# Kernel tuning notes

Measured on AMD Instinct MI355X. Metric: run time of the kernel, lower is better.

## Reference

```python
import jax, jax.numpy as jnp
import numpy as np

N = 8192
IN_FEATS = 256
D = IN_FEATS // 4  # 64, bottleneck dim
HID = 64           # MLP hidden_dim
K_MAX = 9
K_EC = 20
SLOPE = 0.01       # torch LeakyReLU default


def _leaky(x):
    return jnp.where(x >= 0, x, SLOPE * x)


def _knn_idx(f, k):
    # f: [N, d]; returns [N, k] indices of k nearest (incl. self, dist 0), ascending distance
    sq = jnp.sum(f * f, axis=1)
    dist = sq[:, None] + sq[None, :] - 2.0 * (f @ f.T)  # [N, N]
    _, idx = jax.lax.top_k(-dist, k)
    return idx


def _edge_conv(f, idx, Wt, bt, Wp, bp, W1, b1, W2, b2):
    # f: [N, d]; idx: [N, k] neighbor (src) indices; dst is the row node.
    x_nb = f[idx]                                   # [N, k, d] gather of src feats
    theta = (f[:, None, :] - x_nb) @ Wt.T + bt      # v_sub_u -> theta Linear
    phi = f @ Wp.T + bp                             # [N, d]
    z = phi[:, None, :] + theta                     # [N, k, d]
    # MLP(hidden=64, 2 layers, leaky_relu, activation_first=True)
    z = _leaky(z) @ W1.T + b1
    z = _leaky(z) @ W2.T + b2
    return jnp.max(z, axis=1)                       # max aggregation per dst


def _lin_init(key, out_dim, in_dim):
    k1, k2 = jax.random.split(key)
    bound = 1.0 / np.sqrt(in_dim)
    W = jax.random.uniform(k1, (out_dim, in_dim), jnp.float32, -bound, bound)
    b = jax.random.uniform(k2, (out_dim,), jnp.float32, -bound, bound)
    return W, b


def setup_inputs() -> dict:
    key = jax.random.key(0)
    keys = jax.random.split(key, 12)
    inp = {"feature": jax.random.normal(keys[0], (N, IN_FEATS), jnp.float32)}
    inp["Wb"], inp["bb"] = _lin_init(keys[1], D, IN_FEATS)
    inp["Wt1"], inp["bt1"] = _lin_init(keys[2], D, D)
    inp["Wp1"], inp["bp1"] = _lin_init(keys[3], D, D)
    inp["Wm1a"], inp["bm1a"] = _lin_init(keys[4], HID, D)
    inp["Wm1b"], inp["bm1b"] = _lin_init(keys[5], D, HID)
    inp["Wt2"], inp["bt2"] = _lin_init(keys[6], D, D)
    inp["Wp2"], inp["bp2"] = _lin_init(keys[7], D, D)
    inp["Wm2a"], inp["bm2a"] = _lin_init(keys[8], HID, D)
    inp["Wm2b"], inp["bm2b"] = _lin_init(keys[9], D, HID)
    inp["Wl"], inp["bl"] = _lin_init(keys[10], IN_FEATS, 3 * D)
    return inp


def reference(feature, Wb, bb, Wt1, bt1, Wp1, bp1, Wm1a, bm1a, Wm1b, bm1b,
              Wt2, bt2, Wp2, bp2, Wm2a, bm2a, Wm2b, bm2b, Wl, bl):
    f = feature @ Wb.T + bb                          # bottleneck [N, D]
    # KNN indices are non-differentiable (torch topk indices) -> stop_gradient
    idx40 = _knn_idx(jax.lax.stop_gradient(f), K_EC * 2)  # 40-NN, ascending distance
    idx9 = idx40[:, :K_MAX]
    idx20 = idx40[:, :K_EC]            # dilation 1
    idx20_d2 = idx40[:, ::2]           # dilation 2: every 2nd of 40-NN
    h_max = jnp.max(f[idx9], axis=1)   # copy_u + max over 9-NN
    h1 = _edge_conv(f, idx20, Wt1, bt1, Wp1, bp1, Wm1a, bm1a, Wm1b, bm1b)
    h2 = _edge_conv(f, idx20_d2, Wt2, bt2, Wp2, bp2, Wm2a, bm2a, Wm2b, bm2b)
    h = jnp.concatenate([h1, h2, h_max], axis=1) @ Wl.T + bl
    return h + feature                 # residual
```

## Files before the change

### kernel.cpp

```cpp
#include <hip/hip_runtime.h>
#include <math.h>

#define NPT   8192
#define FIN   256
#define DD    64
#define KSEL  48
#define QT    16

#define LEAKY(x) (((x) >= 0.f) ? (x) : 0.01f*(x))

using short8v = __attribute__((ext_vector_type(8))) short;
using f32x4   = __attribute__((ext_vector_type(4))) float;

__device__ inline unsigned short f2bf(float x) {
  union { float f; unsigned u; } v; v.f = x;
  unsigned r = v.u + 0x7fff + ((v.u >> 16) & 1);
  return (unsigned short)(r >> 16);
}
__device__ inline float bf2f(unsigned short h) {
  union { unsigned u; float f; } v; v.u = ((unsigned)h) << 16; return v.f;
}

__device__ __forceinline__ void sort_merge(float& ld, int& li, float sd, int si, int l) {
  #pragma unroll
  for (int k = 2; k <= 64; k <<= 1) {
    #pragma unroll
    for (int j = k >> 1; j >= 1; j >>= 1) {
      float pd = __shfl_xor(sd, j);
      int   pi = __shfl_xor(si, j);
      bool up = ((l & k) == 0);
      bool lower = ((l & j) == 0);
      bool takeMin = (up == lower);
      bool pick = takeMin ? (pd < sd) : (pd > sd);
      sd = pick ? pd : sd;
      si = pick ? pi : si;
    }
  }
  float rd = __shfl(sd, 63 - l);
  int   ri = __shfl(si, 63 - l);
  bool keep = (ld <= rd);
  float md = keep ? ld : rd;
  int   mi = keep ? li : ri;
  #pragma unroll
  for (int j = 32; j >= 1; j >>= 1) {
    float pd = __shfl_xor(md, j);
    int   pi = __shfl_xor(mi, j);
    bool lower = ((l & j) == 0);
    bool pick = lower ? (pd < md) : (pd > md);
    md = pick ? pd : md;
    mi = pick ? pi : mi;
  }
  ld = md; li = mi;
}

__global__ void k0_prep(const float* __restrict__ Wl, const float* __restrict__ Wb,
                        const float* __restrict__ Wt1, const float* __restrict__ Wp1,
                        const float* __restrict__ Wt2, const float* __restrict__ Wp2,
                        float* __restrict__ WlT, float* __restrict__ WbT,
                        float* __restrict__ WtT1, float* __restrict__ WpT1,
                        float* __restrict__ WtT2, float* __restrict__ WpT2)
{
  const int b = blockIdx.x, t = threadIdx.x;
  if (b < 192) {
    WlT[b*256 + t] = Wl[t*192 + b];
  } else if (b < 256) {
    int j = (b - 192)*4 + (t >> 6), o = t & 63;
    WbT[j*64 + o] = Wb[o*256 + j];
  } else {
    int m = b - 256;
    const float* src = (m==0) ? Wt1 : (m==1) ? Wp1 : (m==2) ? Wt2 : Wp2;
    float*       dst = (m==0) ? WtT1: (m==1) ? WpT1: (m==2) ? WtT2: WpT2;
    #pragma unroll
    for (int i = 0; i < 16; ++i) {
      int idx = t + 256*i, r = idx >> 6, c = idx & 63;
      dst[c*64 + r] = src[r*64 + c];
    }
  }
}

__global__ __launch_bounds__(256) void k1_precompute(
    const float* __restrict__ feature, const float* __restrict__ WbT, const float* __restrict__ bb,
    const float* __restrict__ WtT1, const float* __restrict__ bt1,
    const float* __restrict__ WpT1, const float* __restrict__ bp1,
    const float* __restrict__ WtT2, const float* __restrict__ bt2,
    const float* __restrict__ WpT2, const float* __restrict__ bp2,
    double* __restrict__ f64d, double* __restrict__ sq64,
    float* __restrict__ f32v, float* __restrict__ sqf,
    float* __restrict__ u1, float* __restrict__ c1,
    float* __restrict__ u2, float* __restrict__ c2)
{
  __shared__ float f_s[4*64];
  const int w = threadIdx.x >> 6, l = threadIdx.x & 63;
  const int i = blockIdx.x*4 + w;
  const float* frow = feature + i*FIN;
  double facc = (double)bb[l];
  #pragma unroll 4
  for (int j = 0; j < FIN; ++j)
    facc += (double)frow[j] * (double)WbT[j*64 + l];
  f64d[i*DD + l] = facc;
  float f32 = (float)facc;
  f32v[i*DD + l] = f32;
  double s = facc*facc;
  #pragma unroll
  for (int off = 32; off; off >>= 1) s += __shfl_xor(s, off);
  if (l == 0) { sq64[i] = s; sqf[i] = (float)s; }
  f_s[w*64 + l] = f32;
  float au1 = 0.f, ap1 = 0.f, au2 = 0.f, ap2 = 0.f;
  for (int e = 0; e < DD; ++e) {
    float fe = f_s[w*64 + e];
    au1 += fe * WtT1[e*64 + l];
    ap1 += fe * WpT1[e*64 + l];
    au2 += fe * WtT2[e*64 + l];
    ap2 += fe * WpT2[e*64 + l];
  }
  u1[i*DD+l] = au1;
  c1[i*DD+l] = ap1 + bp1[l] + au1 + bt1[l];
  u2[i*DD+l] = au2;
  c2[i*DD+l] = ap2 + bp2[l] + au2 + bt2[l];
}

__global__ __launch_bounds__(256) void k1b_frag(
    const float* __restrict__ f32v,
    unsigned short* __restrict__ Saf, unsigned short* __restrict__ Sbf)
{
  const int w = threadIdx.x >> 6, l = threadIdx.x & 63;
  const int task = blockIdx.x*4 + w;
  const int tile = task / 6, ks = task % 6;
  const int row  = tile*16 + (l & 15);
  const int inner = (ks & 1)*32 + ((l >> 4) << 3);
  union { unsigned short u[8]; short8v v; } pa, pb;
  #pragma unroll
  for (int j = 0; j < 8; ++j) {
    float x = f32v[row*64 + inner + j];
    unsigned short hi = f2bf(x);
    unsigned short lo = f2bf(x - bf2f(hi));
    pa.u[j] = (ks < 4) ? hi : lo;
    pb.u[j] = (ks < 2) ? hi : ((ks < 4) ? lo : hi);
  }
  size_t off = ((size_t)(tile*6 + ks)*64 + l)*8;
  *(short8v*)&Saf[off] = pa.v;
  *(short8v*)&Sbf[off] = pb.v;
}

__global__ __launch_bounds__(256) void k1c_wfrag(
    const float* __restrict__ Wm1a, const float* __restrict__ Wm1b,
    const float* __restrict__ Wm2a, const float* __restrict__ Wm2b,
    unsigned short* __restrict__ F1a, unsigned short* __restrict__ F1b,
    unsigned short* __restrict__ F2a, unsigned short* __restrict__ F2b)
{
  const int w = threadIdx.x >> 6, l = threadIdx.x & 63;
  const int task = blockIdx.x*4 + w;
  const int which = task / 24, rem = task % 24;
  const int nt = rem / 6, ks = rem % 6;
  const float* W = (which==0) ? Wm1a : (which==1) ? Wm1b : (which==2) ? Wm2a : Wm2b;
  unsigned short* F = (which==0) ? F1a : (which==1) ? F1b : (which==2) ? F2a : F2b;
  const int row = nt*16 + (l & 15);
  const int inner = (ks & 1)*32 + ((l >> 4) << 3);
  union { unsigned short u[8]; short8v v; } p;
  #pragma unroll
  for (int j = 0; j < 8; ++j) {
    float x = W[row*64 + inner + j];
    unsigned short hi = f2bf(x);
    unsigned short lo = f2bf(x - bf2f(hi));
    p.u[j] = (ks < 2) ? hi : ((ks < 4) ? lo : hi);
  }
  *(short8v*)&F[((size_t)(nt*6 + ks)*64 + l)*8] = p.v;
}

__global__ __launch_bounds__(512) void k2_knn(
    const unsigned short* __restrict__ Saf,
    const unsigned short* __restrict__ Sbf,
    const float* __restrict__ sqf,
    int* __restrict__ idx48)
{
  __shared__ float dist_s[2][QT*132];
  __shared__ float buf_d[8*2*64];
  __shared__ int   buf_i[8*2*64];

  const int t = threadIdx.x;
  const int w = t >> 6, l = t & 63;
  const int qbase = blockIdx.x * QT;

  short8v afr[4];
  {
    const size_t b = (size_t)blockIdx.x*6;
    afr[0] = *(const short8v*)&Saf[((b+0)*64 + l)*8];
    afr[1] = *(const short8v*)&Saf[((b+1)*64 + l)*8];
    afr[2] = *(const short8v*)&Saf[((b+4)*64 + l)*8];
    afr[3] = *(const short8v*)&Saf[((b+5)*64 + l)*8];
  }
  short8v bfr[4];
  {
    const size_t b = (size_t)w*6;
    #pragma unroll
    for (int s = 0; s < 4; ++s)
      bfr[s] = *(const short8v*)&Sbf[((b+s)*64 + l)*8];
  }

  float ld[2] = {__builtin_inff(), __builtin_inff()};
  int   li[2] = {0, 0};
  float thr[2] = {__builtin_inff(), __builtin_inff()};
  int   bc[2] = {0, 0};

  for (int cb = 0; cb < NPT/128; ++cb) {
    const int jbase = cb*128;
    const float sc = sqf[jbase + w*16 + (l & 15)];
    f32x4 acc = {0.f, 0.f, 0.f, 0.f};
    acc = __builtin_amdgcn_mfma_f32_16x16x32_bf16(afr[0], bfr[0], acc, 0, 0, 0);
    acc = __builtin_amdgcn_mfma_f32_16x16x32_bf16(afr[1], bfr[1], acc, 0, 0, 0);
    acc = __builtin_amdgcn_mfma_f32_16x16x32_bf16(afr[0], bfr[2], acc, 0, 0, 0);
    acc = __builtin_amdgcn_mfma_f32_16x16x32_bf16(afr[1], bfr[3], acc, 0, 0, 0);
    acc = __builtin_amdgcn_mfma_f32_16x16x32_bf16(afr[2], bfr[0], acc, 0, 0, 0);
    acc = __builtin_amdgcn_mfma_f32_16x16x32_bf16(afr[3], bfr[1], acc, 0, 0, 0);
    if (cb < NPT/128 - 1) {
      const size_t b = (size_t)((cb+1)*8 + w)*6;
      #pragma unroll
      for (int s = 0; s < 4; ++s)
        bfr[s] = *(const short8v*)&Sbf[((b+s)*64 + l)*8];
    }
    {
      const int ncol = w*16 + (l & 15);
      #pragma unroll
      for (int r = 0; r < 4; ++r) {
        const int qrow = ((l >> 4)*4) + r;
        dist_s[cb&1][qrow*132 + ncol] = sc - 2.0f*acc[r];
      }
    }
    __syncthreads();
    #pragma unroll
    for (int qq = 0; qq < 2; ++qq) {
      const int q = 2*w + qq;
      float* bufd = &buf_d[(w*2 + qq)*64];
      int*   bufi = &buf_i[(w*2 + qq)*64];
      #pragma unroll
      for (int half = 0; half < 2; ++half) {
        float d = dist_s[cb&1][q*132 + 64*half + l];
        bool pass = d < thr[qq];
        unsigned long long m = __ballot(pass);
        if (m) {
          int cnt = __popcll(m);
          int bco = bc[qq];
          if (bco + cnt > 64) {
            float sd = (l < bco) ? bufd[l] : __builtin_inff();
            int   si = (l < bco) ? bufi[l] : 0;
            sort_merge(ld[qq], li[qq], sd, si, l);
            thr[qq] = __shfl(ld[qq], 47);
            bco = 0;
          }
          if (pass) {
            int slot = bco + __popcll(m & ((1ull << l) - 1ull));
            bufd[slot] = d;
            bufi[slot] = jbase + 64*half + l;
          }
          bc[qq] = bco + cnt;
        }
      }
    }
  }
  #pragma unroll
  for (int qq = 0; qq < 2; ++qq) {
    const int q = 2*w + qq;
    if (bc[qq] > 0) {
      float* bufd = &buf_d[(w*2 + qq)*64];
      int*   bufi = &buf_i[(w*2 + qq)*64];
      float sd = (l < bc[qq]) ? bufd[l] : __builtin_inff();
      int   si = (l < bc[qq]) ? bufi[l] : 0;
      sort_merge(ld[qq], li[qq], sd, si, l);
    }
    if (l < KSEL) idx48[(qbase + q)*KSEL + l] = li[qq];
  }
}

__global__ __launch_bounds__(256) void k2b_rerank(
    const double* __restrict__ f64d, const double* __restrict__ sq64,
    const int* __restrict__ idx48, int* __restrict__ idx40)
{
  __shared__ double sbd[4*KSEL];
  __shared__ int    sbi[4*KSEL];
  const int w = threadIdx.x >> 6, l = threadIdx.x & 63;
  const int node = blockIdx.x*4 + w;
  double dm = 0.0; int cand = 0;
  if (l < KSEL) {
    cand = idx48[node*KSEL + l];
    const double* fi = f64d + node*DD;
    const double* fc = f64d + (long)cand*DD;
    double acc = 0.0;
    #pragma unroll 8
    for (int d = 0; d < DD; ++d) acc += fi[d]*fc[d];
    dm = sq64[node] + sq64[cand] - 2.0*acc;
    sbd[w*KSEL + l] = dm; sbi[w*KSEL + l] = cand;
  }
  __syncthreads();
  if (l < KSEL) {
    int rank = 0;
    for (int j = 0; j < KSEL; ++j) {
      double dj = sbd[w*KSEL + j];
      int    ij = sbi[w*KSEL + j];
      rank += (dj < dm) || (dj == dm && ij < cand);
    }
    if (rank < 40) idx40[node*40 + rank] = cand;
  }
}

__device__ __forceinline__ void build_frags(const float* __restrict__ zs, int mt, int l,
                                            short8v fr[4]) {
  const int row = mt*16 + (l & 15);
  const int base = row*68 + ((l >> 4) << 3);
  union { unsigned short u[8]; short8v v; } h0, h1, q0, q1;
  #pragma unroll
  for (int j = 0; j < 8; ++j) {
    float x0 = zs[base + j];
    float x1 = zs[base + 32 + j];
    unsigned short a = f2bf(x0);
    unsigned short b = f2bf(x1);
    h0.u[j] = a; q0.u[j] = f2bf(x0 - bf2f(a));
    h1.u[j] = b; q1.u[j] = f2bf(x1 - bf2f(b));
  }
  fr[0] = h0.v; fr[1] = h1.v; fr[2] = q0.v; fr[3] = q1.v;
}

#define MFMA6(ACC, AF, W0, W1, W2, W3)                                          \
  ACC = __builtin_amdgcn_mfma_f32_16x16x32_bf16(AF[0], W0, ACC, 0, 0, 0);       \
  ACC = __builtin_amdgcn_mfma_f32_16x16x32_bf16(AF[1], W1, ACC, 0, 0, 0);       \
  ACC = __builtin_amdgcn_mfma_f32_16x16x32_bf16(AF[0], W2, ACC, 0, 0, 0);       \
  ACC = __builtin_amdgcn_mfma_f32_16x16x32_bf16(AF[1], W3, ACC, 0, 0, 0);       \
  ACC = __builtin_amdgcn_mfma_f32_16x16x32_bf16(AF[2], W0, ACC, 0, 0, 0);       \
  ACC = __builtin_amdgcn_mfma_f32_16x16x32_bf16(AF[3], W1, ACC, 0, 0, 0);

__global__ __launch_bounds__(256) void k3_edgeconv(
    const float* __restrict__ f32v,
    const float* __restrict__ u1, const float* __restrict__ c1,
    const float* __restrict__ u2, const float* __restrict__ c2,
    const unsigned short* __restrict__ F1a, const unsigned short* __restrict__ F1b,
    const unsigned short* __restrict__ F2a, const unsigned short* __restrict__ F2b,
    const float* __restrict__ bm1a, const float* __restrict__ bm1b,
    const float* __restrict__ bm2a, const float* __restrict__ bm2b,
    const int* __restrict__ idx40, float* __restrict__ hout)
{
  __shared__ __align__(16) float z_s[32*68];
  __shared__ __align__(16) float a_s[32*68];
  __shared__ float red_s[2*64];
  __shared__ int idx_sh[40];
  const int t = threadIdx.x, i = blockIdx.x;
  const int w = t >> 6, l = t & 63;
  const int mt = w >> 1;
  const int nb0 = (w & 1)*2;
  if (t < 40) idx_sh[t] = idx40[i*40 + t];
  __syncthreads();

  for (int conv = 0; conv < 2; ++conv) {
    const float* u_g = conv ? u2 : u1;
    const float* c_g = conv ? c2 : c1;
    const unsigned short* WfA = conv ? F2a : F1a;
    const unsigned short* WfB = conv ? F2b : F1b;
    const float* bav = conv ? bm2a : bm1a;
    const float* bbv = conv ? bm2b : bm1b;
    #pragma unroll
    for (int r = 0; r < 8; ++r) {
      int flat = t + 256*r, row = flat >> 6, d = flat & 63;
      float z = 0.f;
      if (row < 20) {
        int nb = idx_sh[conv ? 2*row : row];
        float zv = c_g[i*DD + d] - u_g[nb*DD + d];
        z = LEAKY(zv);
      }
      z_s[row*68 + d] = z;
    }
    __syncthreads();
    short8v afr[4];
    build_frags(z_s, mt, l, afr);
    f32x4 acc0 = {0.f,0.f,0.f,0.f}, acc1 = {0.f,0.f,0.f,0.f};
    {
      const unsigned short* p0 = WfA + ((size_t)(nb0+0)*6*64)*8;
      const unsigned short* p1 = WfA + ((size_t)(nb0+1)*6*64)*8;
      short8v w00 = *(const short8v*)&p0[(0*64+l)*8];
      short8v w01 = *(const short8v*)&p0[(1*64+l)*8];
      short8v w02 = *(const short8v*)&p0[(2*64+l)*8];
      short8v w03 = *(const short8v*)&p0[(3*64+l)*8];
      short8v w10 = *(const short8v*)&p1[(0*64+l)*8];
      short8v w11 = *(const short8v*)&p1[(1*64+l)*8];
      short8v w12 = *(const short8v*)&p1[(2*64+l)*8];
      short8v w13 = *(const short8v*)&p1[(3*64+l)*8];
      MFMA6(acc0, afr, w00, w01, w02, w03);
      MFMA6(acc1, afr, w10, w11, w12, w13);
    }
    {
      const int c0 = (nb0+0)*16 + (l & 15), c1i = (nb0+1)*16 + (l & 15);
      const float ba0 = bav[c0], ba1 = bav[c1i];
      #pragma unroll
      for (int r = 0; r < 4; ++r) {
        const int row = mt*16 + (l >> 4)*4 + r;
        float v0 = acc0[r] + ba0;
        float v1 = acc1[r] + ba1;
        a_s[row*68 + c0]  = LEAKY(v0);
        a_s[row*68 + c1i] = LEAKY(v1);
      }
    }
    __syncthreads();
    short8v bfr[4];
    build_frags(a_s, mt, l, bfr);
    f32x4 bacc0 = {0.f,0.f,0.f,0.f}, bacc1 = {0.f,0.f,0.f,0.f};
    {
      const unsigned short* p0 = WfB + ((size_t)(nb0+0)*6*64)*8;
      const unsigned short* p1 = WfB + ((size_t)(nb0+1)*6*64)*8;
      short8v w00 = *(const short8v*)&p0[(0*64+l)*8];
      short8v w01 = *(const short8v*)&p0[(1*64+l)*8];
      short8v w02 = *(const short8v*)&p0[(2*64+l)*8];
      short8v w03 = *(const short8v*)&p0[(3*64+l)*8];
      short8v w10 = *(const short8v*)&p1[(0*64+l)*8];
      short8v w11 = *(const short8v*)&p1[(1*64+l)*8];
      short8v w12 = *(const short8v*)&p1[(2*64+l)*8];
      short8v w13 = *(const short8v*)&p1[(3*64+l)*8];
      MFMA6(bacc0, bfr, w00, w01, w02, w03);
      MFMA6(bacc1, bfr, w10, w11, w12, w13);
    }
    {
      const int c0 = (nb0+0)*16 + (l & 15), c1i = (nb0+1)*16 + (l & 15);
      const float bb0 = bbv[c0], bb1 = bbv[c1i];
      float m0 = -__builtin_inff(), m1 = -__builtin_inff();
      #pragma unroll
      for (int r = 0; r < 4; ++r) {
        const int row = mt*16 + (l >> 4)*4 + r;
        if (row < 20) {
          m0 = fmaxf(m0, bacc0[r] + bb0);
          m1 = fmaxf(m1, bacc1[r] + bb1);
        }
      }
      m0 = fmaxf(m0, __shfl_xor(m0, 16)); m0 = fmaxf(m0, __shfl_xor(m0, 32));
      m1 = fmaxf(m1, __shfl_xor(m1, 16)); m1 = fmaxf(m1, __shfl_xor(m1, 32));
      if ((l >> 4) == 0) {
        red_s[mt*64 + c0]  = m0;
        red_s[mt*64 + c1i] = m1;
      }
    }
    __syncthreads();
    if (t < 64) hout[i*192 + conv*64 + t] = fmaxf(red_s[t], red_s[64 + t]);
    __syncthreads();
  }
  if (t < 64) {
    float m = -__builtin_inff();
    #pragma unroll
    for (int k = 0; k < 9; ++k) m = fmaxf(m, f32v[idx_sh[k]*DD + t]);
    hout[i*192 + 128 + t] = m;
  }
}

__global__ __launch_bounds__(256) void k4_final(
    const float* __restrict__ hbuf, const float* __restrict__ WlT,
    const float* __restrict__ bl, const float* __restrict__ feature,
    float* __restrict__ out)
{
  __shared__ __align__(16) float h_sh[16*192];
  const int t = threadIdx.x;
  const int nbase = blockIdx.x * 16;
  #pragma unroll
  for (int r = 0; r < 3; ++r) {
    int flat = t + 256*r;
    int n = flat / 48, j4 = flat % 48;
    *(float4*)&h_sh[n*192 + 4*j4] = *(const float4*)&hbuf[(nbase+n)*192 + 4*j4];
  }
  __syncthreads();
  float acc[16];
  #pragma unroll
  for (int n = 0; n < 16; ++n) acc[n] = 0.f;
  for (int j4 = 0; j4 < 48; ++j4) {
    float w0 = WlT[(4*j4+0)*256 + t];
    float w1 = WlT[(4*j4+1)*256 + t];
    float w2 = WlT[(4*j4+2)*256 + t];
    float w3 = WlT[(4*j4+3)*256 + t];
    #pragma unroll
    for (int n = 0; n < 16; ++n) {
      float4 hv = *(const float4*)&h_sh[n*192 + 4*j4];
      acc[n] += hv.x*w0 + hv.y*w1 + hv.z*w2 + hv.w*w3;
    }
  }
  float blv = bl[t];
  #pragma unroll
  for (int n = 0; n < 16; ++n)
    out[(nbase+n)*256 + t] = acc[n] + blv + feature[(nbase+n)*256 + t];
}

extern "C" void kernel_launch(void* const* d_in, const int* in_sizes, int n_in,
                              void* d_out, int out_size, void* d_ws, size_t ws_size,
                              hipStream_t stream) {
  const float* feature = (const float*)d_in[0];
  const float* Wb   = (const float*)d_in[1];
  const float* bb   = (const float*)d_in[2];
  const float* Wt1  = (const float*)d_in[3];
  const float* bt1  = (const float*)d_in[4];
  const float* Wp1  = (const float*)d_in[5];
  const float* bp1  = (const float*)d_in[6];
  const float* Wm1a = (const float*)d_in[7];
  const float* bm1a = (const float*)d_in[8];
  const float* Wm1b = (const float*)d_in[9];
  const float* bm1b = (const float*)d_in[10];
  const float* Wt2  = (const float*)d_in[11];
  const float* bt2  = (const float*)d_in[12];
  const float* Wp2  = (const float*)d_in[13];
  const float* bp2  = (const float*)d_in[14];
  const float* Wm2a = (const float*)d_in[15];
  const float* bm2a = (const float*)d_in[16];
  const float* Wm2b = (const float*)d_in[17];
  const float* bm2b = (const float*)d_in[18];
  const float* Wl   = (const float*)d_in[19];
  const float* bl   = (const float*)d_in[20];
  float* out = (float*)d_out;

  char* ws = (char*)d_ws;
  double* f64d = (double*)(ws + 0);
  double* sq64 = (double*)(ws + 4194304);
  float*  f32v = (float*)(ws + 4259840);
  float*  sqf  = (float*)(ws + 6356992);
  float*  u1   = (float*)(ws + 6389760);
  float*  c1   = (float*)(ws + 8486912);
  float*  u2   = (float*)(ws + 10584064);
  float*  c2   = (float*)(ws + 12681216);
  int*    idx48= (int*)(ws + 14778368);
  int*    idx40= (int*)(ws + 16351232);
  float*  hbuf = (float*)(ws + 17661952);
  float*  WlT  = (float*)(ws + 23953408);
  unsigned short* Saf = (unsigned short*)(ws + 24150016);
  unsigned short* Sbf = (unsigned short*)(ws + 27295744);
  float*  WbT  = (float*)(ws + 30441472);
  float*  WtT1 = (float*)(ws + 30507008);
  float*  WpT1 = (float*)(ws + 30523392);
  float*  WtT2 = (float*)(ws + 30539776);
  float*  WpT2 = (float*)(ws + 30556160);
  unsigned short* F1a = (unsigned short*)(ws + 30572544);
  unsigned short* F1b = (unsigned short*)(ws + 30597120);
  unsigned short* F2a = (unsigned short*)(ws + 30621696);
  unsigned short* F2b = (unsigned short*)(ws + 30646272);

  hipLaunchKernelGGL(k0_prep, dim3(260), dim3(256), 0, stream,
                     Wl, Wb, Wt1, Wp1, Wt2, Wp2, WlT, WbT, WtT1, WpT1, WtT2, WpT2);
  hipLaunchKernelGGL(k1c_wfrag, dim3(24), dim3(256), 0, stream,
                     Wm1a, Wm1b, Wm2a, Wm2b, F1a, F1b, F2a, F2b);
  hipLaunchKernelGGL(k1_precompute, dim3(2048), dim3(256), 0, stream,
                     feature, WbT, bb, WtT1, bt1, WpT1, bp1, WtT2, bt2, WpT2, bp2,
                     f64d, sq64, f32v, sqf, u1, c1, u2, c2);
  hipLaunchKernelGGL(k1b_frag, dim3(768), dim3(256), 0, stream, f32v, Saf, Sbf);
  hipLaunchKernelGGL(k2_knn, dim3(NPT/QT), dim3(512), 0, stream, Saf, Sbf, sqf, idx48);
  hipLaunchKernelGGL(k2b_rerank, dim3(2048), dim3(256), 0, stream, f64d, sq64, idx48, idx40);
  hipLaunchKernelGGL(k3_edgeconv, dim3(8192), dim3(256), 0, stream,
                     f32v, u1, c1, u2, c2, F1a, F1b, F2a, F2b,
                     bm1a, bm1b, bm2a, bm2b, idx40, hbuf);
  hipLaunchKernelGGL(k4_final, dim3(512), dim3(256), 0, stream, hbuf, WlT, bl, feature, out);
}
```

Measured before the change: 437.8 us.

## Split KNN candidate scan into two halves and rerank merged 96 candidates

The KNN kernel now launches twice as many blocks, each scanning half of the candidate columns and keeping its own top-48, which gives more parallelism across CUs. The rerank kernel then merges the 96 candidates per node in double precision, with 128 threads per node. The bottleneck precompute loop is also rewritten to use float4 loads and four independent double accumulators, and the workspace layout is compacted so hbuf aliases the now-dead Saf buffer. The cost is a larger rerank with more candidates per node and a quadratic rank computation.

```diff
diff --git a/kernel.cpp b/kernel.cpp
--- a/kernel.cpp
+++ b/kernel.cpp
@@ -93,10 +93,16 @@
   const int w = threadIdx.x >> 6, l = threadIdx.x & 63;
   const int i = blockIdx.x*4 + w;
   const float* frow = feature + i*FIN;
-  double facc = (double)bb[l];
-  #pragma unroll 4
-  for (int j = 0; j < FIN; ++j)
-    facc += (double)frow[j] * (double)WbT[j*64 + l];
+  double a0 = (double)bb[l], a1 = 0.0, a2 = 0.0, a3 = 0.0;
+  #pragma unroll 2
+  for (int j = 0; j < FIN; j += 4) {
+    float4 fv = *(const float4*)&frow[j];
+    a0 += (double)fv.x * (double)WbT[(j+0)*64 + l];
+    a1 += (double)fv.y * (double)WbT[(j+1)*64 + l];
+    a2 += (double)fv.z * (double)WbT[(j+2)*64 + l];
+    a3 += (double)fv.w * (double)WbT[(j+3)*64 + l];
+  }
+  double facc = (a0 + a1) + (a2 + a3);
   f64d[i*DD + l] = facc;
   float f32 = (float)facc;
   f32v[i*DD + l] = f32;
@@ -171,7 +177,7 @@
     const unsigned short* __restrict__ Saf,
     const unsigned short* __restrict__ Sbf,
     const float* __restrict__ sqf,
-    int* __restrict__ idx48)
+    int* __restrict__ idx96)
 {
   __shared__ float dist_s[2][QT*132];
   __shared__ float buf_d[8*2*64];
@@ -179,11 +185,14 @@
 
   const int t = threadIdx.x;
   const int w = t >> 6, l = t & 63;
-  const int qbase = blockIdx.x * QT;
+  const int qb = blockIdx.x & 511;
+  const int half = blockIdx.x >> 9;
+  const int qbase = qb * QT;
+  const int ctile0 = half * 256;
 
   short8v afr[4];
   {
-    const size_t b = (size_t)blockIdx.x*6;
+    const size_t b = (size_t)qb*6;
     afr[0] = *(const short8v*)&Saf[((b+0)*64 + l)*8];
     afr[1] = *(const short8v*)&Saf[((b+1)*64 + l)*8];
     afr[2] = *(const short8v*)&Saf[((b+4)*64 + l)*8];
@@ -191,7 +200,7 @@
   }
   short8v bfr[4];
   {
-    const size_t b = (size_t)w*6;
+    const size_t b = (size_t)(ctile0 + w)*6;
     #pragma unroll
     for (int s = 0; s < 4; ++s)
       bfr[s] = *(const short8v*)&Sbf[((b+s)*64 + l)*8];
@@ -202,8 +211,8 @@
   float thr[2] = {__builtin_inff(), __builtin_inff()};
   int   bc[2] = {0, 0};
 
-  for (int cb = 0; cb < NPT/128; ++cb) {
-    const int jbase = cb*128;
+  for (int cb = 0; cb < 32; ++cb) {
+    const int jbase = half*4096 + cb*128;
     const float sc = sqf[jbase + w*16 + (l & 15)];
     f32x4 acc = {0.f, 0.f, 0.f, 0.f};
     acc = __builtin_amdgcn_mfma_f32_16x16x32_bf16(afr[0], bfr[0], acc, 0, 0, 0);
@@ -212,8 +221,8 @@
     acc = __builtin_amdgcn_mfma_f32_16x16x32_bf16(afr[1], bfr[3], acc, 0, 0, 0);
     acc = __builtin_amdgcn_mfma_f32_16x16x32_bf16(afr[2], bfr[0], acc, 0, 0, 0);
     acc = __builtin_amdgcn_mfma_f32_16x16x32_bf16(afr[3], bfr[1], acc, 0, 0, 0);
-    if (cb < NPT/128 - 1) {
-      const size_t b = (size_t)((cb+1)*8 + w)*6;
+    if (cb < 31) {
+      const size_t b = (size_t)(ctile0 + (cb+1)*8 + w)*6;
       #pragma unroll
       for (int s = 0; s < 4; ++s)
         bfr[s] = *(const short8v*)&Sbf[((b+s)*64 + l)*8];
@@ -233,8 +242,8 @@
       float* bufd = &buf_d[(w*2 + qq)*64];
       int*   bufi = &buf_i[(w*2 + qq)*64];
       #pragma unroll
-      for (int half = 0; half < 2; ++half) {
-        float d = dist_s[cb&1][q*132 + 64*half + l];
+      for (int hh = 0; hh < 2; ++hh) {
+        float d = dist_s[cb&1][q*132 + 64*hh + l];
         bool pass = d < thr[qq];
         unsigned long long m = __ballot(pass);
         if (m) {
@@ -250,7 +259,7 @@
           if (pass) {
             int slot = bco + __popcll(m & ((1ull << l) - 1ull));
             bufd[slot] = d;
-            bufi[slot] = jbase + 64*half + l;
+            bufi[slot] = jbase + 64*hh + l;
           }
           bc[qq] = bco + cnt;
         }
@@ -267,35 +276,36 @@
       int   si = (l < bc[qq]) ? bufi[l] : 0;
       sort_merge(ld[qq], li[qq], sd, si, l);
     }
-    if (l < KSEL) idx48[(qbase + q)*KSEL + l] = li[qq];
+    if (l < KSEL) idx96[(qbase + q)*96 + half*KSEL + l] = li[qq];
   }
 }
 
 __global__ __launch_bounds__(256) void k2b_rerank(
     const double* __restrict__ f64d, const double* __restrict__ sq64,
-    const int* __restrict__ idx48, int* __restrict__ idx40)
-{
-  __shared__ double sbd[4*KSEL];
-  __shared__ int    sbi[4*KSEL];
-  const int w = threadIdx.x >> 6, l = threadIdx.x & 63;
-  const int node = blockIdx.x*4 + w;
+    const int* __restrict__ idx96, int* __restrict__ idx40)
+{
+  __shared__ double sbd[2*96];
+  __shared__ int    sbi[2*96];
+  const int sub = threadIdx.x >> 7;
+  const int c = threadIdx.x & 127;
+  const int node = blockIdx.x*2 + sub;
   double dm = 0.0; int cand = 0;
-  if (l < KSEL) {
-    cand = idx48[node*KSEL + l];
-    const double* fi = f64d + node*DD;
-    const double* fc = f64d + (long)cand*DD;
-    double acc = 0.0;
+  if (c < 96) {
+    cand = idx96[node*96 + c];
+    const double* fi = f64d + (size_t)node*DD;
+    const double* fc = f64d + (size_t)cand*DD;
+    double a0 = 0.0, a1 = 0.0;
     #pragma unroll 8
-    for (int d = 0; d < DD; ++d) acc += fi[d]*fc[d];
-    dm = sq64[node] + sq64[cand] - 2.0*acc;
-    sbd[w*KSEL + l] = dm; sbi[w*KSEL + l] = cand;
+    for (int d = 0; d < DD; d += 2) { a0 += fi[d]*fc[d]; a1 += fi[d+1]*fc[d+1]; }
+    dm = sq64[node] + sq64[cand] - 2.0*(a0 + a1);
+    sbd[sub*96 + c] = dm; sbi[sub*96 + c] = cand;
   }
   __syncthreads();
-  if (l < KSEL) {
+  if (c < 96) {
     int rank = 0;
-    for (int j = 0; j < KSEL; ++j) {
-      double dj = sbd[w*KSEL + j];
-      int    ij = sbi[w*KSEL + j];
+    for (int j = 0; j < 96; ++j) {
+      double dj = sbd[sub*96 + j];
+      int    ij = sbi[sub*96 + j];
       rank += (dj < dm) || (dj == dm && ij < cand);
     }
     if (rank < 40) idx40[node*40 + rank] = cand;
@@ -515,21 +525,21 @@
   float*  c1   = (float*)(ws + 8486912);
   float*  u2   = (float*)(ws + 10584064);
   float*  c2   = (float*)(ws + 12681216);
-  int*    idx48= (int*)(ws + 14778368);
-  int*    idx40= (int*)(ws + 16351232);
-  float*  hbuf = (float*)(ws + 17661952);
-  float*  WlT  = (float*)(ws + 23953408);
-  unsigned short* Saf = (unsigned short*)(ws + 24150016);
-  unsigned short* Sbf = (unsigned short*)(ws + 27295744);
-  float*  WbT  = (float*)(ws + 30441472);
-  float*  WtT1 = (float*)(ws + 30507008);
-  float*  WpT1 = (float*)(ws + 30523392);
-  float*  WtT2 = (float*)(ws + 30539776);
-  float*  WpT2 = (float*)(ws + 30556160);
-  unsigned short* F1a = (unsigned short*)(ws + 30572544);
-  unsigned short* F1b = (unsigned short*)(ws + 30597120);
-  unsigned short* F2a = (unsigned short*)(ws + 30621696);
-  unsigned short* F2b = (unsigned short*)(ws + 30646272);
+  int*    idx96= (int*)(ws + 14778368);
+  int*    idx40= (int*)(ws + 17924096);
+  unsigned short* Saf = (unsigned short*)(ws + 19234816);
+  unsigned short* Sbf = (unsigned short*)(ws + 22380544);
+  float*  hbuf = (float*)(ws + 19234816);
+  float*  WlT  = (float*)(ws + 25526272);
+  float*  WbT  = (float*)(ws + 25722880);
+  float*  WtT1 = (float*)(ws + 25788416);
+  float*  WpT1 = (float*)(ws + 25804800);
+  float*  WtT2 = (float*)(ws + 25821184);
+  float*  WpT2 = (float*)(ws + 25837568);
+  unsigned short* F1a = (unsigned short*)(ws + 25853952);
+  unsigned short* F1b = (unsigned short*)(ws + 25878528);
+  unsigned short* F2a = (unsigned short*)(ws + 25903104);
+  unsigned short* F2b = (unsigned short*)(ws + 25927680);
 
   hipLaunchKernelGGL(k0_prep, dim3(260), dim3(256), 0, stream,
                      Wl, Wb, Wt1, Wp1, Wt2, Wp2, WlT, WbT, WtT1, WpT1, WtT2, WpT2);
@@ -539,8 +549,8 @@
                      feature, WbT, bb, WtT1, bt1, WpT1, bp1, WtT2, bt2, WpT2, bp2,
                      f64d, sq64, f32v, sqf, u1, c1, u2, c2);
   hipLaunchKernelGGL(k1b_frag, dim3(768), dim3(256), 0, stream, f32v, Saf, Sbf);
-  hipLaunchKernelGGL(k2_knn, dim3(NPT/QT), dim3(512), 0, stream, Saf, Sbf, sqf, idx48);
-  hipLaunchKernelGGL(k2b_rerank, dim3(2048), dim3(256), 0, stream, f64d, sq64, idx48, idx40);
+  hipLaunchKernelGGL(k2_knn, dim3(1024), dim3(512), 0, stream, Saf, Sbf, sqf, idx96);
+  hipLaunchKernelGGL(k2b_rerank, dim3(4096), dim3(256), 0, stream, f64d, sq64, idx96, idx40);
   hipLaunchKernelGGL(k3_edgeconv, dim3(8192), dim3(256), 0, stream,
                      f32v, u1, c1, u2, c2, F1a, F1b, F2a, F2b,
                      bm1a, bm1b, bm2a, bm2b, idx40, hbuf);
```

After: 523.8 us. 1.2x slower.

## Replace bitonic sort-merge in KNN with radix-select over larger candidate buffer

Applied to the files above, without the earlier changes.

The KNN candidate buffer per query grows from 64 to 128 entries, and each flush now runs a wave-wide 32-bit radix select that keeps the 48 smallest keys unsorted, replacing the bitonic sort and merge. The final output is unordered and relies on the rerank kernel to order the candidates. The bottleneck matvec now uses float4 loads with four independent double accumulators, and the rerank dot product is split across two accumulators to shorten dependency chains. The radix select costs 32 ballot rounds per flush and raises shared memory use, a trade against fewer, cheaper flushes than the bitonic network needed.

```diff
diff --git a/kernel.cpp b/kernel.cpp
--- a/kernel.cpp
+++ b/kernel.cpp
@@ -6,6 +6,7 @@
 #define DD    64
 #define KSEL  48
 #define QT    16
+#define BCAP  128
 
 #define LEAKY(x) (((x) >= 0.f) ? (x) : 0.01f*(x))
 
@@ -20,37 +21,54 @@
 __device__ inline float bf2f(unsigned short h) {
   union { unsigned u; float f; } v; v.u = ((unsigned)h) << 16; return v.f;
 }
-
-__device__ __forceinline__ void sort_merge(float& ld, int& li, float sd, int si, int l) {
-  #pragma unroll
-  for (int k = 2; k <= 64; k <<= 1) {
-    #pragma unroll
-    for (int j = k >> 1; j >= 1; j >>= 1) {
-      float pd = __shfl_xor(sd, j);
-      int   pi = __shfl_xor(si, j);
-      bool up = ((l & k) == 0);
-      bool lower = ((l & j) == 0);
-      bool takeMin = (up == lower);
-      bool pick = takeMin ? (pd < sd) : (pd > sd);
-      sd = pick ? pd : sd;
-      si = pick ? pi : si;
-    }
-  }
-  float rd = __shfl(sd, 63 - l);
-  int   ri = __shfl(si, 63 - l);
-  bool keep = (ld <= rd);
-  float md = keep ? ld : rd;
-  int   mi = keep ? li : ri;
-  #pragma unroll
-  for (int j = 32; j >= 1; j >>= 1) {
-    float pd = __shfl_xor(md, j);
-    int   pi = __shfl_xor(mi, j);
-    bool lower = ((l & j) == 0);
-    bool pick = lower ? (pd < md) : (pd > md);
-    md = pick ? pd : md;
-    mi = pick ? pi : mi;
-  }
-  ld = md; li = mi;
+__device__ inline unsigned key_of(float f) {
+  unsigned u = __float_as_uint(f);
+  return (u & 0x80000000u) ? ~u : (u | 0x80000000u);
+}
+__device__ inline float key_inv(unsigned k) {
+  unsigned u = (k >> 31) ? (k ^ 0x80000000u) : ~k;
+  return __uint_as_float(u);
+}
+
+__device__ __attribute__((noinline)) void select48(
+    float* __restrict__ bufd, int* __restrict__ bufi,
+    int l, int n, int* bc, float* thr)
+{
+  float d0 = bufd[l];
+  float d1 = bufd[64 + l];
+  int   i0 = bufi[l];
+  int   i1 = bufi[64 + l];
+  unsigned k0 = (l < n)      ? key_of(d0) : 0xFFFFFFFFu;
+  unsigned k1 = (64 + l < n) ? key_of(d1) : 0xFFFFFFFFu;
+  unsigned prefix = 0; int need = KSEL;
+  #pragma unroll
+  for (int b = 31; b >= 0; --b) {
+    unsigned p2 = prefix << 1;
+    int c = __popcll(__ballot((k0 >> b) == p2)) +
+            __popcll(__ballot((k1 >> b) == p2));
+    if (c >= need) prefix = p2; else { prefix = p2 | 1u; need -= c; }
+  }
+  unsigned long long blt0 = __ballot(k0 < prefix), blt1 = __ballot(k1 < prefix);
+  unsigned long long beq0 = __ballot(k0 == prefix), beq1 = __ballot(k1 == prefix);
+  const int s = __popcll(blt0) + __popcll(blt1);
+  const int tneed = KSEL - s;
+  const unsigned long long below = (1ull << l) - 1ull;
+  if (k0 < prefix) {
+    int dst = __popcll(blt0 & below);
+    bufd[dst] = d0; bufi[dst] = i0;
+  } else if (k0 == prefix) {
+    int r = __popcll(beq0 & below);
+    if (r < tneed) { bufd[s + r] = d0; bufi[s + r] = i0; }
+  }
+  if (k1 < prefix) {
+    int dst = __popcll(blt0) + __popcll(blt1 & below);
+    bufd[dst] = d1; bufi[dst] = i1;
+  } else if (k1 == prefix) {
+    int r = __popcll(beq0) + __popcll(beq1 & below);
+    if (r < tneed) { bufd[s + r] = d1; bufi[s + r] = i1; }
+  }
+  *bc = KSEL;
+  *thr = key_inv(prefix);
 }
 
 __global__ void k0_prep(const float* __restrict__ Wl, const float* __restrict__ Wb,
@@ -93,10 +111,16 @@
   const int w = threadIdx.x >> 6, l = threadIdx.x & 63;
   const int i = blockIdx.x*4 + w;
   const float* frow = feature + i*FIN;
-  double facc = (double)bb[l];
-  #pragma unroll 4
-  for (int j = 0; j < FIN; ++j)
-    facc += (double)frow[j] * (double)WbT[j*64 + l];
+  double a0 = (double)bb[l], a1 = 0.0, a2 = 0.0, a3 = 0.0;
+  #pragma unroll 2
+  for (int j = 0; j < FIN; j += 4) {
+    float4 fv = *(const float4*)&frow[j];
+    a0 += (double)fv.x * (double)WbT[(j+0)*64 + l];
+    a1 += (double)fv.y * (double)WbT[(j+1)*64 + l];
+    a2 += (double)fv.z * (double)WbT[(j+2)*64 + l];
+    a3 += (double)fv.w * (double)WbT[(j+3)*64 + l];
+  }
+  double facc = (a0 + a1) + (a2 + a3);
   f64d[i*DD + l] = facc;
   float f32 = (float)facc;
   f32v[i*DD + l] = f32;
@@ -174,8 +198,8 @@
     int* __restrict__ idx48)
 {
   __shared__ float dist_s[2][QT*132];
-  __shared__ float buf_d[8*2*64];
-  __shared__ int   buf_i[8*2*64];
+  __shared__ float buf_d[QT*BCAP];
+  __shared__ int   buf_i[QT*BCAP];
 
   const int t = threadIdx.x;
   const int w = t >> 6, l = t & 63;
@@ -197,8 +221,6 @@
       bfr[s] = *(const short8v*)&Sbf[((b+s)*64 + l)*8];
   }
 
-  float ld[2] = {__builtin_inff(), __builtin_inff()};
-  int   li[2] = {0, 0};
   float thr[2] = {__builtin_inff(), __builtin_inff()};
   int   bc[2] = {0, 0};
 
@@ -230,29 +252,29 @@
     #pragma unroll
     for (int qq = 0; qq < 2; ++qq) {
       const int q = 2*w + qq;
-      float* bufd = &buf_d[(w*2 + qq)*64];
-      int*   bufi = &buf_i[(w*2 + qq)*64];
+      float* bufd = &buf_d[q*BCAP];
+      int*   bufi = &buf_i[q*BCAP];
+      float dA = dist_s[cb&1][q*132 + l];
+      float dB = dist_s[cb&1][q*132 + 64 + l];
       #pragma unroll
       for (int half = 0; half < 2; ++half) {
-        float d = dist_s[cb&1][q*132 + 64*half + l];
+        float d = half ? dB : dA;
         bool pass = d < thr[qq];
         unsigned long long m = __ballot(pass);
         if (m) {
           int cnt = __popcll(m);
-          int bco = bc[qq];
-          if (bco + cnt > 64) {
-            float sd = (l < bco) ? bufd[l] : __builtin_inff();
-            int   si = (l < bco) ? bufi[l] : 0;
-            sort_merge(ld[qq], li[qq], sd, si, l);
-            thr[qq] = __shfl(ld[qq], 47);
-            bco = 0;
+          if (bc[qq] + cnt > BCAP) {
+            select48(bufd, bufi, l, bc[qq], &bc[qq], &thr[qq]);
+            pass = d < thr[qq];
+            m = __ballot(pass);
+            cnt = __popcll(m);
           }
           if (pass) {
-            int slot = bco + __popcll(m & ((1ull << l) - 1ull));
+            int slot = bc[qq] + __popcll(m & ((1ull << l) - 1ull));
             bufd[slot] = d;
             bufi[slot] = jbase + 64*half + l;
           }
-          bc[qq] = bco + cnt;
+          bc[qq] += cnt;
         }
       }
     }
@@ -260,14 +282,10 @@
   #pragma unroll
   for (int qq = 0; qq < 2; ++qq) {
     const int q = 2*w + qq;
-    if (bc[qq] > 0) {
-      float* bufd = &buf_d[(w*2 + qq)*64];
-      int*   bufi = &buf_i[(w*2 + qq)*64];
-      float sd = (l < bc[qq]) ? bufd[l] : __builtin_inff();
-      int   si = (l < bc[qq]) ? bufi[l] : 0;
-      sort_merge(ld[qq], li[qq], sd, si, l);
-    }
-    if (l < KSEL) idx48[(qbase + q)*KSEL + l] = li[qq];
+    float* bufd = &buf_d[q*BCAP];
+    int*   bufi = &buf_i[q*BCAP];
+    if (bc[qq] > KSEL) select48(bufd, bufi, l, bc[qq], &bc[qq], &thr[qq]);
+    if (l < KSEL) idx48[(qbase + q)*KSEL + l] = bufi[l];
   }
 }
 
@@ -282,12 +300,12 @@
   double dm = 0.0; int cand = 0;
   if (l < KSEL) {
     cand = idx48[node*KSEL + l];
-    const double* fi = f64d + node*DD;
-    const double* fc = f64d + (long)cand*DD;
-    double acc = 0.0;
+    const double* fi = f64d + (size_t)node*DD;
+    const double* fc = f64d + (size_t)cand*DD;
+    double a0 = 0.0, a1 = 0.0;
     #pragma unroll 8
-    for (int d = 0; d < DD; ++d) acc += fi[d]*fc[d];
-    dm = sq64[node] + sq64[cand] - 2.0*acc;
+    for (int d = 0; d < DD; d += 2) { a0 += fi[d]*fc[d]; a1 += fi[d+1]*fc[d+1]; }
+    dm = sq64[node] + sq64[cand] - 2.0*(a0 + a1);
     sbd[w*KSEL + l] = dm; sbi[w*KSEL + l] = cand;
   }
   __syncthreads();
```

Result: slower. 451.2 us (+3.1%).
